# Performance work log

Measured on AMD Instinct MI355X. Metric: run time of the kernel, lower is better.

## Reference

```python
import jax, jax.numpy as jnp
import numpy as np

B, S, D = 4, 2048, 2048
H, K = 16, 128          # num_heads, intermediate_dim
FINAL = H * K           # 2048
VDIM = 2048             # vector_dim
EPS_LN = 1e-6
EPS_NORM = 1e-30


def setup_inputs() -> dict:
    key = jax.random.key(0)
    ks = jax.random.split(key, 8)
    x = jax.random.normal(ks[0], (B, S, D), dtype=jnp.float32)
    vector = jax.random.normal(ks[1], (B, VDIM), dtype=jnp.float32)
    W_att = jax.random.normal(ks[2], (D, H), dtype=jnp.float32) / np.sqrt(D)
    temperature = jnp.ones((1, 1, H), dtype=jnp.float32)
    W_values = jax.random.normal(ks[3], (D, H, K), dtype=jnp.float32) / np.sqrt(D)
    W_op = jax.random.normal(ks[4], (FINAL, VDIM), dtype=jnp.float32) / np.sqrt(FINAL)
    ff1 = jax.random.normal(ks[5], (VDIM + D, D), dtype=jnp.float32) / np.sqrt(VDIM + D)
    ff1_b = jnp.zeros((1, 1, D), dtype=jnp.float32)
    ff2 = jax.random.normal(ks[6], (D, D), dtype=jnp.float32) / np.sqrt(D)
    ff2_b = jnp.zeros((1, 1, D), dtype=jnp.float32)
    gamma = jnp.ones((D,), dtype=jnp.float32)
    beta = jnp.zeros((D,), dtype=jnp.float32)
    return {"x": x, "vector": vector, "W_att": W_att, "temperature": temperature,
            "W_values": W_values, "W_op": W_op, "ff1": ff1, "ff1_b": ff1_b,
            "ff2": ff2, "ff2_b": ff2_b, "gamma": gamma, "beta": beta}


def reference(x, vector, W_att, temperature, W_values, W_op, ff1, ff1_b, ff2, ff2_b, gamma, beta):
    b, s, d = x.shape
    # attention gate per (query) position -- [B,S,H]
    logits = jnp.matmul(x, W_att)
    logits = logits - jnp.max(logits, axis=-2, keepdims=True)
    w = jnp.exp(logits * temperature)
    # exact collapse of repeat+tril+normalize: A[b,i,j,h] = w[b,i,h]*tril[i,j]
    # denom[b,i,h] = w[b,i,h]*(i+1) + 1e-30  ->  out = coef * causal cumsum of v
    counts = jnp.arange(1, s + 1, dtype=x.dtype)[None, :, None]  # [1,S,1]
    coef = w / (w * counts + EPS_NORM)                            # [B,S,H]
    v = jnp.einsum('bsi,ihk->bshk', x, W_values)                  # [B,S,H,K]
    cum_v = jnp.cumsum(v, axis=1)                                 # prefix-sum over keys
    pooled = (coef[..., None] * cum_v).reshape(b, s, -1)          # [B,S,H*K]
    op = jnp.matmul(pooled, W_op) + vector[:, None, :]            # [B,S,VDIM]
    concat = jnp.concatenate([x, op], axis=-1)                    # [B,S,VDIM+D]
    h = jax.nn.relu(jnp.matmul(concat, ff1) + ff1_b)
    h = jax.nn.relu(jnp.matmul(h, ff2) + ff2_b)
    res = h + x
    mean = jnp.mean(res, axis=-1, keepdims=True)
    cen = res - mean
    var = jnp.mean(cen * cen, axis=-1, keepdims=True)
    return cen / jnp.sqrt(var + EPS_LN) * gamma + beta
```

## Files before the change

kernel.cpp:

```cpp
#include <hip/hip_runtime.h>
#include <stdint.h>

#define B_DIM 4
#define S_DIM 2048
#define D_DIM 2048
#define H_DIM 16
#define M_ROWS (B_DIM * S_DIM)
#define CONCAT_LD 4096
#define NCHUNK 32
#define CHLEN (S_DIM / NCHUNK)

#define BM 128
#define BN 128
#define BK 64

typedef __attribute__((ext_vector_type(8))) __bf16 bf16x8;
typedef __attribute__((ext_vector_type(4))) float f32x4;

__device__ inline unsigned short f2bf(float f) {
  union { float f; unsigned u; } x; x.f = f;
  unsigned r = x.u + 0x7fffu + ((x.u >> 16) & 1u);
  return (unsigned short)(r >> 16);
}
__device__ inline float bf2f(unsigned short s) {
  union { unsigned u; float f; } x; x.u = ((unsigned)s) << 16;
  return x.f;
}

__global__ __launch_bounds__(256) void xconv_logits_kernel(
    const float* __restrict__ x, const float* __restrict__ Watt,
    unsigned short* __restrict__ concat, float* __restrict__ logits) {
  int row = blockIdx.x, t = threadIdx.x;
  const float* xr = x + (size_t)row * D_DIM;
  unsigned short* cr = concat + (size_t)row * CONCAT_LD;
  float p[H_DIM];
#pragma unroll
  for (int h = 0; h < H_DIM; ++h) p[h] = 0.f;
#pragma unroll
  for (int i = 0; i < 8; ++i) {
    int k = t + i * 256;
    float xv = xr[k];
    cr[k] = f2bf(xv);
    const float* wr = Watt + (size_t)k * H_DIM;
#pragma unroll
    for (int h = 0; h < H_DIM; ++h) p[h] += xv * wr[h];
  }
  __shared__ float red[4][H_DIM];
  int l = t & 63, w = t >> 6;
#pragma unroll
  for (int h = 0; h < H_DIM; ++h) {
    float v = p[h];
    for (int off = 32; off; off >>= 1) v += __shfl_down(v, off);
    if (l == 0) red[w][h] = v;
  }
  __syncthreads();
  if (t < H_DIM)
    logits[(size_t)row * H_DIM + t] = red[0][t] + red[1][t] + red[2][t] + red[3][t];
}

__global__ __launch_bounds__(256) void transpose_conv_kernel(
    const float* __restrict__ src, unsigned short* __restrict__ dst,
    int R, int C, int ldd) {
  __shared__ float tile[32][33];
  int c0 = blockIdx.x * 32, r0 = blockIdx.y * 32;
  int tx = threadIdx.x & 31, ty = threadIdx.x >> 5;
#pragma unroll
  for (int i = 0; i < 32; i += 8)
    tile[ty + i][tx] = src[(size_t)(r0 + ty + i) * C + c0 + tx];
  __syncthreads();
#pragma unroll
  for (int i = 0; i < 32; i += 8)
    dst[(size_t)(c0 + ty + i) * ldd + r0 + tx] = f2bf(tile[tx][ty + i]);
}

__global__ __launch_bounds__(256) void convert_kernel(
    const float* __restrict__ src, unsigned short* __restrict__ dst) {
  int idx = (blockIdx.x * 256 + threadIdx.x) * 4;
  const float4 v = *(const float4*)(src + idx);
  ushort4 o;
  o.x = f2bf(v.x); o.y = f2bf(v.y); o.z = f2bf(v.z); o.w = f2bf(v.w);
  *(ushort4*)(dst + idx) = o;
}

__global__ __launch_bounds__(256) void coef_kernel(
    const float* __restrict__ logits, const float* __restrict__ temp, float* __restrict__ coef) {
  int b = blockIdx.x >> 4, h = blockIdx.x & 15;
  int t = threadIdx.x;
  const float* lg = logits + (size_t)b * S_DIM * H_DIM + h;
  float mx = -1e30f;
  for (int s = t; s < S_DIM; s += 256) mx = fmaxf(mx, lg[(size_t)s * H_DIM]);
  for (int off = 32; off; off >>= 1) mx = fmaxf(mx, __shfl_down(mx, off));
  __shared__ float red[4];
  if ((t & 63) == 0) red[t >> 6] = mx;
  __syncthreads();
  mx = fmaxf(fmaxf(red[0], red[1]), fmaxf(red[2], red[3]));
  float T = temp[h];
  float* cf = coef + (size_t)b * S_DIM * H_DIM + h;
  for (int s = t; s < S_DIM; s += 256) {
    float w = expf((lg[(size_t)s * H_DIM] - mx) * T);
    cf[(size_t)s * H_DIM] = w / (w * (float)(s + 1) + 1e-30f);
  }
}

__global__ __launch_bounds__(256) void bias2_partial_kernel(
    const float* __restrict__ vector, const float* __restrict__ ff1,
    float* __restrict__ part) {
  int n = blockIdx.x * 256 + threadIdx.x;
  int seg = blockIdx.y, b = blockIdx.z;
  const float* vr = vector + (size_t)b * 2048 + seg * 128;
  const float* fr = ff1 + (size_t)(2048 + seg * 128) * 2048 + n;
  float acc = 0.f;
#pragma unroll 8
  for (int j = 0; j < 128; ++j) acc += vr[j] * fr[(size_t)j * 2048];
  part[((size_t)seg * 4 + b) * 2048 + n] = acc;
}

__global__ __launch_bounds__(256) void bias2_reduce_kernel(
    const float* __restrict__ part, const float* __restrict__ ff1_b,
    float* __restrict__ bias2) {
  int n = blockIdx.x * 256 + threadIdx.x;
  int b = blockIdx.y;
  float acc = ff1_b[n];
#pragma unroll
  for (int s = 0; s < 16; ++s) acc += part[((size_t)s * 4 + b) * 2048 + n];
  bias2[(size_t)b * 2048 + n] = acc;
}

template <int MODE>
__global__ __launch_bounds__(256) void gemm_bt_kernel(
    const unsigned short* __restrict__ A, int lda,
    const unsigned short* __restrict__ Bt, int ldb, int K,
    void* __restrict__ outp, int ldo,
    const float* __restrict__ bias, const float* __restrict__ resid) {
  __shared__ unsigned short As[BM * BK];
  __shared__ unsigned short Bs[BN * BK];
  const int t = threadIdx.x;
  const int w = t >> 6, l = t & 63;
  const int wm = w & 1, wn = w >> 1;
  const int q = l >> 4, ln = l & 15;

  const int L = blockIdx.y * 16 + blockIdx.x;
  const int xcd = L & 7;
  const int W = L >> 3;
  const int bx = W & 15;
  const int by = (W >> 4) * 8 + xcd;
  const int m0 = by * BM, n0 = bx * BN;

  f32x4 acc[4][4];
#pragma unroll
  for (int i = 0; i < 4; ++i)
#pragma unroll
    for (int j = 0; j < 4; ++j) acc[i][j] = {0.f, 0.f, 0.f, 0.f};

  for (int k0 = 0; k0 < K; k0 += BK) {
    __syncthreads();
#pragma unroll
    for (int r = 0; r < 4; ++r) {
      int s = r * 256 + t;
      int row = s >> 3;
      int ch = (s & 7) ^ (row & 7);
      const unsigned short* ga = A + (size_t)(m0 + row) * lda + k0 + ch * 8;
      __builtin_amdgcn_global_load_lds(
          (const __attribute__((address_space(1))) void*)ga,
          (__attribute__((address_space(3))) void*)(As + (r * 256 + w * 64) * 8), 16, 0, 0);
      const unsigned short* gb = Bt + (size_t)(n0 + row) * ldb + k0 + ch * 8;
      __builtin_amdgcn_global_load_lds(
          (const __attribute__((address_space(1))) void*)gb,
          (__attribute__((address_space(3))) void*)(Bs + (r * 256 + w * 64) * 8), 16, 0, 0);
    }
    __syncthreads();
#pragma unroll
    for (int h = 0; h < 2; ++h) {
      bf16x8 af[4], bfr[4];
#pragma unroll
      for (int mt = 0; mt < 4; ++mt) {
        int ar = wm * 64 + mt * 16 + ln;
        af[mt] = *(const bf16x8*)&As[ar * BK + (((h * 4 + q) ^ (ar & 7)) * 8)];
      }
#pragma unroll
      for (int nt = 0; nt < 4; ++nt) {
        int br = wn * 64 + nt * 16 + ln;
        bfr[nt] = *(const bf16x8*)&Bs[br * BK + (((h * 4 + q) ^ (br & 7)) * 8)];
      }
#pragma unroll
      for (int mt = 0; mt < 4; ++mt)
#pragma unroll
        for (int nt = 0; nt < 4; ++nt)
          acc[mt][nt] = __builtin_amdgcn_mfma_f32_16x16x32_bf16(af[mt], bfr[nt], acc[mt][nt], 0, 0, 0);
    }
  }

#pragma unroll
  for (int mt = 0; mt < 4; ++mt) {
#pragma unroll
    for (int i = 0; i < 4; ++i) {
      int row = m0 + wm * 64 + mt * 16 + q * 4 + i;
#pragma unroll
      for (int nt = 0; nt < 4; ++nt) {
        int col = n0 + wn * 64 + nt * 16 + ln;
        float vv = acc[mt][nt][i];
        if (MODE == 2) { vv += bias[(size_t)(row >> 11) * 2048 + col]; vv = fmaxf(vv, 0.f); }
        if (MODE == 4) {
          vv += bias[col]; vv = fmaxf(vv, 0.f);
          vv += resid[(size_t)row * 2048 + col];
          ((float*)outp)[(size_t)row * ldo + col] = vv;
        } else {
          ((unsigned short*)outp)[(size_t)row * ldo + col] = f2bf(vv);
        }
      }
    }
  }
}

#define GLD16(g, s)                                                        \
  __builtin_amdgcn_global_load_lds(                                        \
      (const __attribute__((address_space(1))) void*)(g),                  \
      (__attribute__((address_space(3))) void*)(s), 16, 0, 0)
#define BARX() asm volatile("s_barrier" ::: "memory")
#define VMW8() asm volatile("s_waitcnt vmcnt(8)" ::: "memory")
#define VMW0() asm volatile("s_waitcnt vmcnt(0)" ::: "memory")

template <int MODE>
__global__ __launch_bounds__(512, 2) void gemm256_kernel(
    const unsigned short* __restrict__ A, int lda,
    const unsigned short* __restrict__ Bt, int ldb, int K,
    void* __restrict__ outp, int ldo,
    const float* __restrict__ bias, const float* __restrict__ resid) {
  __shared__ unsigned short As[2][2][256 * 32];
  __shared__ unsigned short Bs[2][2][256 * 32];
  const int t = threadIdx.x;
  const int wv = t >> 6, l = t & 63;
  const int wm = wv >> 2, wn = wv & 3;
  const int q = l >> 4, ln = l & 15;

  const int L = blockIdx.y * 8 + blockIdx.x;
  const int lin = (L & 7) * 32 + (L >> 3);
  const int m0 = (lin >> 3) * 256, n0 = (lin & 7) * 256;

  const int srow = t >> 2;
  const int scol = (((t & 3) * 16) ^ (((srow >> 1) & 3) << 4)) >> 1;
  const unsigned short* Abase = A + (size_t)(m0 + srow) * lda + scol;
  const unsigned short* Bbase = Bt + (size_t)(n0 + srow) * ldb + scol;
  const size_t astep = (size_t)128 * lda, bstep = (size_t)128 * ldb;
  const int axor = ((ln >> 1) & 3) << 3;

  f32x4 acc[8][4];
#pragma unroll
  for (int i = 0; i < 8; ++i)
#pragma unroll
    for (int j = 0; j < 4; ++j) acc[i][j] = {0.f, 0.f, 0.f, 0.f};

  auto stageA = [&](int kt, int kh, int buf) {
    const unsigned short* g = Abase + (size_t)kt * 64 + kh * 32;
    GLD16(g, &As[buf][kh][wv * 512]);
    GLD16(g + astep, &As[buf][kh][4096 + wv * 512]);
  };
  auto stageB = [&](int kt, int kh, int buf) {
    const unsigned short* g = Bbase + (size_t)kt * 64 + kh * 32;
    GLD16(g, &Bs[buf][kh][wv * 512]);
    GLD16(g + bstep, &Bs[buf][kh][4096 + wv * 512]);
  };

  bf16x8 a[8], b[2];
  auto loadA = [&](int buf, int h) {
#pragma unroll
    for (int mt = 0; mt < 8; ++mt) {
      int ar = wm * 128 + mt * 16 + ln;
      a[mt] = *(const bf16x8*)&As[buf][h][ar * 32 + ((q * 8) ^ axor)];
    }
  };
  auto loadB2 = [&](int buf, int h, int np) {
#pragma unroll
    for (int i = 0; i < 2; ++i) {
      int br = wn * 64 + (np * 2 + i) * 16 + ln;
      b[i] = *(const bf16x8*)&Bs[buf][h][br * 32 + ((q * 8) ^ axor)];
    }
  };
  auto mm = [&](int np) {
    __builtin_amdgcn_s_setprio(1);
#pragma unroll
    for (int mt = 0; mt < 8; ++mt)
#pragma unroll
      for (int i = 0; i < 2; ++i)
        acc[mt][np * 2 + i] =
            __builtin_amdgcn_mfma_f32_16x16x32_bf16(a[mt], b[i], acc[mt][np * 2 + i], 0, 0, 0);
    __builtin_amdgcn_s_setprio(0);
  };

  const int NT = K >> 6;
  stageA(0, 0, 0); stageB(0, 0, 0);
  stageA(0, 1, 0); stageB(0, 1, 0);
  stageA(1, 0, 1); stageB(1, 0, 1);
  VMW8();
  BARX();

  for (int tt = 0; tt < NT; ++tt) {
    const int c = tt & 1;
    const int t1 = (tt + 1 == NT) ? 0 : tt + 1;
    const int t2 = (tt + 2 >= NT) ? tt + 2 - NT : tt + 2;
    loadA(c, 0); loadB2(c, 0, 0);
    stageA(t1, 1, c ^ 1);
    BARX();
    mm(0);
    BARX();
    loadB2(c, 0, 1);
    stageB(t1, 1, c ^ 1);
    BARX();
    mm(1);
    VMW8();
    BARX();
    loadA(c, 1); loadB2(c, 1, 0);
    stageA(t2, 0, c);
    BARX();
    mm(0);
    BARX();
    loadB2(c, 1, 1);
    stageB(t2, 0, c);
    BARX();
    mm(1);
    VMW8();
    BARX();
  }
  VMW0();

#pragma unroll
  for (int mt = 0; mt < 8; ++mt) {
#pragma unroll
    for (int i = 0; i < 4; ++i) {
      int row = m0 + wm * 128 + mt * 16 + q * 4 + i;
#pragma unroll
      for (int nt = 0; nt < 4; ++nt) {
        int col = n0 + wn * 64 + nt * 16 + ln;
        float vv = acc[mt][nt][i];
        if (MODE == 2) { vv += bias[(size_t)(row >> 11) * 2048 + col]; vv = fmaxf(vv, 0.f); }
        if (MODE == 4) {
          vv += bias[col]; vv = fmaxf(vv, 0.f);
          vv += resid[(size_t)row * 2048 + col];
          ((float*)outp)[(size_t)row * ldo + col] = vv;
        } else {
          ((unsigned short*)outp)[(size_t)row * ldo + col] = f2bf(vv);
        }
      }
    }
  }
}

__global__ __launch_bounds__(256) void scan_partial_kernel(
    const unsigned short* __restrict__ v, float* __restrict__ csum) {
  int c = blockIdx.x * 256 + threadIdx.x;
  int chunk = blockIdx.y, b = blockIdx.z;
  const unsigned short* p = v + ((size_t)(b * S_DIM + chunk * CHLEN)) * D_DIM + c;
  float s = 0.f;
#pragma unroll 4
  for (int i = 0; i < CHLEN; ++i) s += bf2f(p[(size_t)i * D_DIM]);
  csum[((size_t)b * NCHUNK + chunk) * D_DIM + c] = s;
}

__global__ __launch_bounds__(256) void scan_offsets_kernel(float* __restrict__ csum) {
  int c = blockIdx.x * 256 + threadIdx.x;
  int b = blockIdx.y;
  float run = 0.f;
  float* p = csum + (size_t)b * NCHUNK * D_DIM + c;
  for (int ch = 0; ch < NCHUNK; ++ch) {
    float tv = p[(size_t)ch * D_DIM];
    p[(size_t)ch * D_DIM] = run;
    run += tv;
  }
}

__global__ __launch_bounds__(256) void scan_apply_kernel(
    const unsigned short* __restrict__ v, const float* __restrict__ csum,
    const float* __restrict__ coef, unsigned short* __restrict__ pooled_out) {
  int c = blockIdx.x * 256 + threadIdx.x;
  int chunk = blockIdx.y, b = blockIdx.z;
  int h = c >> 7;
  int row0 = b * S_DIM + chunk * CHLEN;
  float run = csum[((size_t)b * NCHUNK + chunk) * D_DIM + c];
  const unsigned short* vp = v + (size_t)row0 * D_DIM + c;
  unsigned short* po = pooled_out + (size_t)row0 * CONCAT_LD + c;
  const float* cf = coef + (size_t)row0 * H_DIM + h;
#pragma unroll 4
  for (int i = 0; i < CHLEN; ++i) {
    run += bf2f(vp[(size_t)i * D_DIM]);
    po[(size_t)i * CONCAT_LD] = f2bf(cf[(size_t)i * H_DIM] * run);
  }
}

__global__ __launch_bounds__(256) void ln_kernel(
    float* __restrict__ out, const float* __restrict__ gamma, const float* __restrict__ beta) {
  int row = blockIdx.x, t = threadIdx.x;
  float* pr = out + (size_t)row * D_DIM;
  float vals[8];
  float s = 0.f;
#pragma unroll
  for (int i = 0; i < 8; ++i) { vals[i] = pr[t + i * 256]; s += vals[i]; }
  __shared__ float red[4];
  for (int off = 32; off; off >>= 1) s += __shfl_down(s, off);
  if ((t & 63) == 0) red[t >> 6] = s;
  __syncthreads();
  float mean = (red[0] + red[1] + red[2] + red[3]) * (1.f / D_DIM);
  __syncthreads();
  float c2 = 0.f;
#pragma unroll
  for (int i = 0; i < 8; ++i) { float c = vals[i] - mean; c2 += c * c; }
  for (int off = 32; off; off >>= 1) c2 += __shfl_down(c2, off);
  if ((t & 63) == 0) red[t >> 6] = c2;
  __syncthreads();
  float var = (red[0] + red[1] + red[2] + red[3]) * (1.f / D_DIM);
  float rstd = rsqrtf(var + 1e-6f);
#pragma unroll
  for (int i = 0; i < 8; ++i) {
    int col = t + i * 256;
    pr[col] = (vals[i] - mean) * rstd * gamma[col] + beta[col];
  }
}

extern "C" void kernel_launch(void* const* d_in, const int* in_sizes, int n_in,
                              void* d_out, int out_size, void* d_ws, size_t ws_size,
                              hipStream_t stream) {
  const float* x      = (const float*)d_in[0];
  const float* vector = (const float*)d_in[1];
  const float* W_att  = (const float*)d_in[2];
  const float* temp   = (const float*)d_in[3];
  const float* W_val  = (const float*)d_in[4];
  const float* W_op   = (const float*)d_in[5];
  const float* ff1    = (const float*)d_in[6];
  const float* ff1_b  = (const float*)d_in[7];
  const float* ff2    = (const float*)d_in[8];
  const float* ff2_b  = (const float*)d_in[9];
  const float* gamma  = (const float*)d_in[10];
  const float* beta   = (const float*)d_in[11];
  float* out = (float*)d_out;

  char* ws = (char*)d_ws;
  auto alloc = [&](size_t bytes) {
    char* p = ws; ws += (bytes + 255) & ~(size_t)255; return p;
  };
  unsigned short* concat = (unsigned short*)alloc((size_t)M_ROWS * CONCAT_LD * 2);
  unsigned short* wv_t   = (unsigned short*)alloc((size_t)2048 * 2048 * 2);
  unsigned short* btff1  = (unsigned short*)alloc((size_t)2048 * 4096 * 2);
  unsigned short* f1bT   = (unsigned short*)alloc((size_t)2048 * 2048 * 2);
  unsigned short* wop_bf = (unsigned short*)alloc((size_t)2048 * 2048 * 2);
  unsigned short* ff2_t  = (unsigned short*)alloc((size_t)2048 * 2048 * 2);
  unsigned short* vbuf   = (unsigned short*)alloc((size_t)M_ROWS * 2048 * 2);
  unsigned short* h1     = (unsigned short*)alloc((size_t)M_ROWS * 2048 * 2);
  float* logits = (float*)alloc((size_t)M_ROWS * H_DIM * 4);
  float* coef   = (float*)alloc((size_t)M_ROWS * H_DIM * 4);
  float* csum   = (float*)alloc((size_t)B_DIM * NCHUNK * D_DIM * 4);
  float* part   = (float*)alloc((size_t)16 * 4 * 2048 * 4);
  float* bias2  = (float*)alloc((size_t)4 * 2048 * 4);

  xconv_logits_kernel<<<M_ROWS, 256, 0, stream>>>(x, W_att, concat, logits);
  transpose_conv_kernel<<<dim3(64, 64), 256, 0, stream>>>(W_val, wv_t, 2048, 2048, 2048);
  transpose_conv_kernel<<<dim3(64, 64), 256, 0, stream>>>(ff1, btff1, 2048, 2048, 4096);
  transpose_conv_kernel<<<dim3(64, 64), 256, 0, stream>>>(ff1 + (size_t)2048 * 2048, f1bT, 2048, 2048, 2048);
  convert_kernel<<<2048 * 2048 / 1024, 256, 0, stream>>>(W_op, wop_bf);
  transpose_conv_kernel<<<dim3(64, 64), 256, 0, stream>>>(ff2, ff2_t, 2048, 2048, 2048);
  coef_kernel<<<B_DIM * H_DIM, 256, 0, stream>>>(logits, temp, coef);
  gemm_bt_kernel<1><<<dim3(16, 16), 256, 0, stream>>>(
      f1bT, 2048, wop_bf, 2048, 2048, btff1 + 2048, 4096, nullptr, nullptr);
  bias2_partial_kernel<<<dim3(8, 16, 4), 256, 0, stream>>>(vector, ff1, part);
  bias2_reduce_kernel<<<dim3(8, 4), 256, 0, stream>>>(part, ff1_b, bias2);
  gemm256_kernel<1><<<dim3(8, 32), 512, 0, stream>>>(
      concat, CONCAT_LD, wv_t, 2048, 2048, vbuf, 2048, nullptr, nullptr);
  scan_partial_kernel<<<dim3(8, NCHUNK, B_DIM), 256, 0, stream>>>(vbuf, csum);
  scan_offsets_kernel<<<dim3(8, B_DIM), 256, 0, stream>>>(csum);
  scan_apply_kernel<<<dim3(8, NCHUNK, B_DIM), 256, 0, stream>>>(vbuf, csum, coef, concat + 2048);
  gemm256_kernel<2><<<dim3(8, 32), 512, 0, stream>>>(
      concat, CONCAT_LD, btff1, 4096, 4096, h1, 2048, bias2, nullptr);
  gemm256_kernel<4><<<dim3(8, 32), 512, 0, stream>>>(
      h1, 2048, ff2_t, 2048, 2048, out, 2048, ff2_b, x);
  ln_kernel<<<M_ROWS, 256, 0, stream>>>(out, gamma, beta);
}
```

Before: 664.7 us.

## Double-buffer A/B fragment registers to overlap LDS reads with MFMA

Restructures the GEMM main loop so LDS fragment loads for the next sub-step go into alternate register sets (a0/a1, ba/bb) while MFMAs run on the current set. It prefetches the first fragments before the loop and adjusts the vmcnt waits from 8 to 6 and 4 to match the new count of outstanding global-to-LDS loads. The aim is to hide LDS read latency behind matrix math. In exchange it uses more VGPRs, which could cause spills under launch_bounds(512,2), and the hand-tuned waitcnt values must stay correct or reads may race with the async stages.

```diff
diff --git a/kernel.cpp b/kernel.cpp
--- a/kernel.cpp
+++ b/kernel.cpp
@@ -217,8 +217,36 @@
       (const __attribute__((address_space(1))) void*)(g),                  \
       (__attribute__((address_space(3))) void*)(s), 16, 0, 0)
 #define BARX() asm volatile("s_barrier" ::: "memory")
-#define VMW8() asm volatile("s_waitcnt vmcnt(8)" ::: "memory")
+#define VMW6() asm volatile("s_waitcnt vmcnt(6)" ::: "memory")
+#define VMW4() asm volatile("s_waitcnt vmcnt(4)" ::: "memory")
 #define VMW0() asm volatile("s_waitcnt vmcnt(0)" ::: "memory")
+
+#define LD_A4(areg, base, buf, h)                                          \
+  do {                                                                     \
+    _Pragma("unroll") for (int _i = 0; _i < 4; ++_i) {                     \
+      int ar = wm * 128 + ((base) + _i) * 16 + ln;                         \
+      areg[(base) + _i] = *(const bf16x8*)&As[buf][h][ar * 32 + rsel];     \
+    }                                                                      \
+  } while (0)
+
+#define LD_B2(breg, buf, h, np)                                            \
+  do {                                                                     \
+    _Pragma("unroll") for (int _i = 0; _i < 2; ++_i) {                     \
+      int br = wn * 64 + ((np)*2 + _i) * 16 + ln;                          \
+      breg[_i] = *(const bf16x8*)&Bs[buf][h][br * 32 + rsel];              \
+    }                                                                      \
+  } while (0)
+
+#define MM(areg, breg, np)                                                 \
+  do {                                                                     \
+    __builtin_amdgcn_s_setprio(1);                                         \
+    _Pragma("unroll") for (int _mt = 0; _mt < 8; ++_mt) {                  \
+      _Pragma("unroll") for (int _i = 0; _i < 2; ++_i)                     \
+          acc[_mt][(np)*2 + _i] = __builtin_amdgcn_mfma_f32_16x16x32_bf16( \
+              areg[_mt], breg[_i], acc[_mt][(np)*2 + _i], 0, 0, 0);        \
+    }                                                                      \
+    __builtin_amdgcn_s_setprio(0);                                         \
+  } while (0)
 
 template <int MODE>
 __global__ __launch_bounds__(512, 2) void gemm256_kernel(
@@ -242,7 +270,7 @@
   const unsigned short* Abase = A + (size_t)(m0 + srow) * lda + scol;
   const unsigned short* Bbase = Bt + (size_t)(n0 + srow) * ldb + scol;
   const size_t astep = (size_t)128 * lda, bstep = (size_t)128 * ldb;
-  const int axor = ((ln >> 1) & 3) << 3;
+  const int rsel = (q * 8) ^ (((ln >> 1) & 3) << 3);
 
   f32x4 acc[8][4];
 #pragma unroll
@@ -261,64 +289,49 @@
     GLD16(g + bstep, &Bs[buf][kh][4096 + wv * 512]);
   };
 
-  bf16x8 a[8], b[2];
-  auto loadA = [&](int buf, int h) {
-#pragma unroll
-    for (int mt = 0; mt < 8; ++mt) {
-      int ar = wm * 128 + mt * 16 + ln;
-      a[mt] = *(const bf16x8*)&As[buf][h][ar * 32 + ((q * 8) ^ axor)];
-    }
-  };
-  auto loadB2 = [&](int buf, int h, int np) {
-#pragma unroll
-    for (int i = 0; i < 2; ++i) {
-      int br = wn * 64 + (np * 2 + i) * 16 + ln;
-      b[i] = *(const bf16x8*)&Bs[buf][h][br * 32 + ((q * 8) ^ axor)];
-    }
-  };
-  auto mm = [&](int np) {
-    __builtin_amdgcn_s_setprio(1);
-#pragma unroll
-    for (int mt = 0; mt < 8; ++mt)
-#pragma unroll
-      for (int i = 0; i < 2; ++i)
-        acc[mt][np * 2 + i] =
-            __builtin_amdgcn_mfma_f32_16x16x32_bf16(a[mt], b[i], acc[mt][np * 2 + i], 0, 0, 0);
-    __builtin_amdgcn_s_setprio(0);
-  };
+  bf16x8 a0[8], a1[8], ba[2], bb[2];
 
   const int NT = K >> 6;
   stageA(0, 0, 0); stageB(0, 0, 0);
   stageA(0, 1, 0); stageB(0, 1, 0);
   stageA(1, 0, 1); stageB(1, 0, 1);
-  VMW8();
+  VMW4();
   BARX();
+  LD_A4(a0, 0, 0, 0);
+  LD_A4(a0, 4, 0, 0);
+  LD_B2(ba, 0, 0, 0);
 
   for (int tt = 0; tt < NT; ++tt) {
     const int c = tt & 1;
     const int t1 = (tt + 1 == NT) ? 0 : tt + 1;
     const int t2 = (tt + 2 >= NT) ? tt + 2 - NT : tt + 2;
-    loadA(c, 0); loadB2(c, 0, 0);
+    LD_B2(bb, c, 0, 1);
+    LD_A4(a1, 0, c, 1);
     stageA(t1, 1, c ^ 1);
     BARX();
-    mm(0);
-    BARX();
-    loadB2(c, 0, 1);
+    MM(a0, ba, 0);
+    VMW6();
+    BARX();
+    LD_A4(a1, 4, c, 1);
+    LD_B2(ba, c, 1, 0);
     stageB(t1, 1, c ^ 1);
     BARX();
-    mm(1);
-    VMW8();
-    BARX();
-    loadA(c, 1); loadB2(c, 1, 0);
+    MM(a0, bb, 1);
+    VMW6();
+    BARX();
+    LD_B2(bb, c, 1, 1);
+    LD_A4(a0, 0, c ^ 1, 0);
     stageA(t2, 0, c);
     BARX();
-    mm(0);
-    BARX();
-    loadB2(c, 1, 1);
+    MM(a1, ba, 0);
+    VMW6();
+    BARX();
+    LD_A4(a0, 4, c ^ 1, 0);
+    LD_B2(ba, c ^ 1, 0, 0);
     stageB(t2, 0, c);
     BARX();
-    mm(1);
-    VMW8();
+    MM(a1, bb, 1);
+    VMW6();
     BARX();
   }
   VMW0();
```

Result: slower. 718.4 us (+8.1%).
